# Optimization experiments

Measured on AMD Instinct MI355X. Metric: run time of the kernel, lower is better.

## Reference

```python
import jax, jax.numpy as jnp
import numpy as np

N, E = 50000, 800000
IN, HID, HEADS, OUT, EDIM = 128, 32, 4, 40, 5
HC = HEADS * HID  # 128, conv1 output width


def setup_inputs() -> dict:
    key = jax.random.key(0)
    ks = jax.random.split(key, 24)
    p = lambda i, shape: (jax.random.normal(ks[i], shape, jnp.float32) * 0.1)
    return {
        "x": jax.random.normal(ks[0], (N, IN), jnp.float32),
        "edge_index": jax.random.randint(ks[1], (2, E), 0, N, jnp.int32),
        "edge_attr": jax.random.normal(ks[2], (E, EDIM), jnp.float32),
        # GATConv layer 1 (in -> hidden, heads=4)
        "W1": p(3, (IN, HC)), "att_src1": p(4, (HEADS, HID)), "att_dst1": p(5, (HEADS, HID)),
        "att_edge1": p(6, (HEADS, HID)), "We1": p(7, (EDIM, HC)), "b1": p(8, (HC,)),
        # GATConv layer 2 (hidden*heads -> out, heads=1)
        "W2": p(9, (HC, OUT)), "att_src2": p(10, (1, OUT)), "att_dst2": p(11, (1, OUT)),
        "att_edge2": p(12, (1, OUT)), "We2": p(13, (EDIM, OUT)), "b2": p(14, (OUT,)),
        # BatchNorm (eval mode: running stats)
        "g1": jnp.ones((HC,), jnp.float32), "be1": p(15, (HC,)),
        "rm1": p(16, (HC,)), "rv1": jnp.ones((HC,), jnp.float32),
        "g2": jnp.ones((OUT,), jnp.float32), "be2": p(17, (OUT,)),
        "rm2": p(18, (OUT,)), "rv2": jnp.ones((OUT,), jnp.float32),
    }


def gat_conv(x, src, dst, eattr, W, a_src, a_dst, a_edge, We, b, H, C):
    n = x.shape[0]
    xs = (x @ W).reshape(n, H, C)                       # shared lin for src/dst (PyG)
    alpha_s = jnp.einsum('nhc,hc->nh', xs, a_src)       # [N,H]
    alpha_d = jnp.einsum('nhc,hc->nh', xs, a_dst)       # [N,H]
    e = (eattr @ We).reshape(-1, H, C)                  # [E',H,C]
    alpha_e = jnp.einsum('ehc,hc->eh', e, a_edge)       # [E',H]
    alpha = jax.nn.leaky_relu(alpha_s[src] + alpha_d[dst] + alpha_e, 0.2)
    # segment softmax over incoming edges of each dst node
    amax = jax.ops.segment_max(alpha, dst, num_segments=n)
    ex = jnp.exp(alpha - amax[dst])
    denom = jax.ops.segment_sum(ex, dst, num_segments=n)
    coef = ex / (denom[dst] + 1e-16)                    # [E',H]
    out = jax.ops.segment_sum(xs[src] * coef[:, :, None], dst, num_segments=n)
    return out.reshape(n, H * C) + b                    # concat heads + bias


def batch_norm_eval(x, g, be, rm, rv):
    return g * (x - rm) * jax.lax.rsqrt(rv + 1e-5) + be


def reference(x, edge_index, edge_attr, W1, att_src1, att_dst1, att_edge1, We1, b1,
              W2, att_src2, att_dst2, att_edge2, We2, b2,
              g1, be1, rm1, rv1, g2, be2, rm2, rv2):
    src0, dst0 = edge_index[0], edge_index[1]
    # add self loops with fill_value='mean': loop edge_attr = mean of incoming edge_attr
    cnt = jax.ops.segment_sum(jnp.ones((E,), x.dtype), dst0, num_segments=N)
    loop_attr = jax.ops.segment_sum(edge_attr, dst0, num_segments=N) / jnp.maximum(cnt, 1.0)[:, None]
    loop = jnp.arange(N, dtype=src0.dtype)
    src = jnp.concatenate([src0, loop])
    dst = jnp.concatenate([dst0, loop])
    ea = jnp.concatenate([edge_attr, loop_attr], axis=0)
    # layer 1 (dropout = identity in eval)
    h = gat_conv(x, src, dst, ea, W1, att_src1, att_dst1, att_edge1, We1, b1, HEADS, HID)
    h = jax.nn.elu(batch_norm_eval(h, g1, be1, rm1, rv1))
    # layer 2 (heads=1)
    h = gat_conv(h, src, dst, ea, W2, att_src2, att_dst2, att_edge2, We2, b2, 1, OUT)
    h = batch_norm_eval(h, g2, be2, rm2, rv2)
    return jax.nn.log_softmax(h, axis=1)
```

## Files before the change

kernel.cpp:

```cpp
#include <hip/hip_runtime.h>
#include <hip/hip_bf16.h>

#define NN 50000
#define NE 800000
#define SCAN_NB ((NN + 255) / 256)
#define G1_NB ((NN + 63) / 64)
#define A1_NB ((NN + 3) / 4)

typedef float f32x4_t __attribute__((ext_vector_type(4)));
typedef float f32x2_t __attribute__((ext_vector_type(2)));
typedef short s16x8_t __attribute__((ext_vector_type(8)));

__device__ __forceinline__ unsigned f2bf2(float a, float b) {
    unsigned ua = __float_as_uint(a);
    ua = (ua + 0x7fffu + ((ua >> 16) & 1u)) >> 16;
    unsigned ub = __float_as_uint(b);
    ub = (ub + 0x7fffu + ((ub >> 16) & 1u)) >> 16;
    return ua | (ub << 16);
}
__device__ __forceinline__ float bf_lo(unsigned u) { return __uint_as_float(u << 16); }
__device__ __forceinline__ float bf_hi(unsigned u) { return __uint_as_float(u & 0xffff0000u); }
__device__ __forceinline__ f32x2_t bfpair(unsigned u) {
    return (f32x2_t){__uint_as_float(u << 16), __uint_as_float(u & 0xffff0000u)};
}

__global__ __launch_bounds__(256) void prep_kernel(
    const float* __restrict__ We1, const float* __restrict__ ae1w,
    const float* __restrict__ We2, const float* __restrict__ ae2w,
    const float* __restrict__ W1, const float* __restrict__ W2,
    float* __restrict__ wf1, float* __restrict__ wf2,
    unsigned* __restrict__ w1t, unsigned* __restrict__ w2t,
    int* __restrict__ cnt) {
    int t = threadIdx.x;
    int g = blockIdx.x * 256 + t;
    if (g < NN) cnt[g] = 0;
    if (blockIdx.x != 0) return;
    if (t < 20) {
        int j = t >> 2, h = t & 3;
        float s = 0.f;
        for (int c = 0; c < 32; ++c) s += We1[j * 128 + h * 32 + c] * ae1w[h * 32 + c];
        wf1[j * 4 + h] = s;
    }
    if (t >= 32 && t < 37) {
        int j = t - 32;
        float s = 0.f;
        for (int c = 0; c < 40; ++c) s += We2[j * 40 + c] * ae2w[c];
        wf2[j] = s;
    }
    for (int i = t; i < 128 * 64; i += 256) {
        int c = i >> 6, kp = i & 63;
        w1t[i] = f2bf2(W1[(size_t)(2 * kp) * 128 + c], W1[(size_t)(2 * kp + 1) * 128 + c]);
    }
    for (int i = t; i < 48 * 64; i += 256) {
        int c = i >> 6, kp = i & 63;
        w2t[i] = (c < 40) ? f2bf2(W2[(size_t)(2 * kp) * 40 + c], W2[(size_t)(2 * kp + 1) * 40 + c]) : 0u;
    }
}

__global__ __launch_bounds__(256) void gemm1_count(
    const float* __restrict__ A, const unsigned* __restrict__ w1t,
    unsigned* __restrict__ out, const int* __restrict__ dst0,
    int* __restrict__ cnt, int* __restrict__ rank) {
    int t = threadIdx.x;
    int ebase = blockIdx.x * 1024 + t;
    int e0 = ebase, e1 = ebase + 256, e2 = ebase + 512, e3 = ebase + 768;
    int r0 = 0, r1 = 0, r2 = 0, r3 = 0;
    if (e0 < NE) r0 = atomicAdd(&cnt[dst0[e0]], 1);
    if (e1 < NE) r1 = atomicAdd(&cnt[dst0[e1]], 1);
    if (e2 < NE) r2 = atomicAdd(&cnt[dst0[e2]], 1);
    if (e3 < NE) r3 = atomicAdd(&cnt[dst0[e3]], 1);

    __shared__ unsigned sA[64 * 68];
    __shared__ unsigned sB[128 * 68];
    int row0 = blockIdx.x * 64;
    for (int i = t; i < 64 * 32; i += 256) {
        int r = i >> 5, q = i & 31;
        int gr = row0 + r;
        float4 v = (gr < NN) ? *(const float4*)&A[(size_t)gr * 128 + q * 4]
                             : make_float4(0.f, 0.f, 0.f, 0.f);
        sA[r * 68 + q * 2]     = f2bf2(v.x, v.y);
        sA[r * 68 + q * 2 + 1] = f2bf2(v.z, v.w);
    }
    for (int i = t; i < 128 * 16; i += 256) {
        int c = i >> 4, q = i & 15;
        *(uint4*)&sB[c * 68 + q * 4] = *(const uint4*)&w1t[c * 64 + q * 4];
    }
    __syncthreads();
    int wv = t >> 6, lane = t & 63;
    int lr = lane & 15, kgrp = lane >> 4;
    f32x4_t acc[8];
#pragma unroll
    for (int i = 0; i < 8; ++i) acc[i] = (f32x4_t){0.f, 0.f, 0.f, 0.f};
    int arow = wv * 16 + lr;
#pragma unroll
    for (int kt = 0; kt < 4; ++kt) {
        int kw = kt * 16 + kgrp * 4;
        s16x8_t af = *(const s16x8_t*)&sA[arow * 68 + kw];
#pragma unroll
        for (int tc = 0; tc < 8; ++tc) {
            s16x8_t bf = *(const s16x8_t*)&sB[(tc * 16 + lr) * 68 + kw];
            acc[tc] = __builtin_amdgcn_mfma_f32_16x16x32_bf16(af, bf, acc[tc], 0, 0, 0);
        }
    }
    int orow0 = row0 + wv * 16 + kgrp * 4;
#pragma unroll
    for (int tc = 0; tc < 8; ++tc) {
#pragma unroll
        for (int r = 0; r < 4; ++r) {
            float v = acc[tc][r];
            float other = __shfl_xor(v, 1);
            int gr = orow0 + r;
            if (!(lane & 1) && gr < NN)
                out[(size_t)gr * 64 + tc * 8 + (lr >> 1)] = f2bf2(v, other);
        }
    }
    if (e0 < NE) rank[e0] = r0;
    if (e1 < NE) rank[e1] = r1;
    if (e2 < NE) rank[e2] = r2;
    if (e3 < NE) rank[e3] = r3;
}

__global__ __launch_bounds__(256) void scan1_alpha1(
    const int* __restrict__ cnt, int* __restrict__ off, int* __restrict__ bsum,
    const unsigned* __restrict__ xs1u, const float* __restrict__ asw,
    const float* __restrict__ adw, float* __restrict__ as1, float* __restrict__ ad1) {
    if (blockIdx.x < SCAN_NB) {
        __shared__ int tmp[256];
        int t = threadIdx.x;
        int g = blockIdx.x * 256 + t;
        int v = (g < NN) ? cnt[g] : 0;
        tmp[t] = v;
        __syncthreads();
#pragma unroll
        for (int d = 1; d < 256; d <<= 1) {
            int u = (t >= d) ? tmp[t - d] : 0;
            __syncthreads();
            tmp[t] += u;
            __syncthreads();
        }
        if (g < NN) off[g] = tmp[t] - v;
        if (t == 255) bsum[blockIdx.x] = tmp[255];
        return;
    }
    int wid = ((blockIdx.x - SCAN_NB) * 256 + threadIdx.x) >> 6;
    if (wid >= NN) return;
    int lane = threadIdx.x & 63;
    int c = lane * 2;
    unsigned u = xs1u[(size_t)wid * 64 + lane];
    float vx = bf_lo(u), vy = bf_hi(u);
    float pa = vx * asw[c] + vy * asw[c + 1];
    float pd = vx * adw[c] + vy * adw[c + 1];
#pragma unroll
    for (int d = 8; d >= 1; d >>= 1) {
        pa += __shfl_xor(pa, d, 16);
        pd += __shfl_xor(pd, d, 16);
    }
    if ((lane & 15) == 0) {
        as1[wid * 4 + (lane >> 4)] = pa;
        ad1[wid * 4 + (lane >> 4)] = pd;
    }
}

__global__ __launch_bounds__(256) void scan3_kernel(int* __restrict__ off,
                                                    const int* __restrict__ bsum,
                                                    const int* __restrict__ cnt) {
    __shared__ int tmp[256];
    int t = threadIdx.x;
    int v = (t < SCAN_NB) ? bsum[t] : 0;
    tmp[t] = v;
    __syncthreads();
#pragma unroll
    for (int d = 1; d < 256; d <<= 1) {
        int u = (t >= d) ? tmp[t - d] : 0;
        __syncthreads();
        tmp[t] += u;
        __syncthreads();
    }
    int pre = (blockIdx.x == 0) ? 0 : tmp[blockIdx.x - 1];
    int g = blockIdx.x * 256 + t;
    if (g < NN) {
        int o = off[g] + pre;
        off[g] = o;
        if (g == NN - 1) off[NN] = o + cnt[g];
    }
}

__global__ __launch_bounds__(256) void fill_fold_kernel(
    const int* __restrict__ src0, const int* __restrict__ dst0,
    const float* __restrict__ eattr, const float* __restrict__ wf1,
    const float* __restrict__ wf2, const int* __restrict__ off,
    const int* __restrict__ rank, uint4* __restrict__ epk) {
    int base = blockIdx.x * 1024 + threadIdx.x;
#pragma unroll
    for (int k = 0; k < 4; ++k) {
        int e = base + k * 256;
        if (e >= NE) continue;
        float a[5];
#pragma unroll
        for (int j = 0; j < 5; ++j) a[j] = eattr[(size_t)e * 5 + j];
        float o[4];
#pragma unroll
        for (int h = 0; h < 4; ++h) {
            float s = 0.f;
#pragma unroll
            for (int j = 0; j < 5; ++j) s += a[j] * wf1[j * 4 + h];
            o[h] = s;
        }
        float s2 = 0.f;
#pragma unroll
        for (int j = 0; j < 5; ++j) s2 += a[j] * wf2[j];
        int pos = off[dst0[e]] + rank[e];
        epk[pos] = make_uint4((unsigned)src0[e], f2bf2(o[0], o[1]), f2bf2(o[2], o[3]),
                              __float_as_uint(s2));
    }
}

__global__ __launch_bounds__(256) void gat1_kernel(
    const uint4* __restrict__ epk, const int* __restrict__ off,
    const unsigned* __restrict__ xs1u,
    const float4* __restrict__ as1, const float4* __restrict__ ad1,
    const float* __restrict__ b1, const float* __restrict__ g1, const float* __restrict__ be1,
    const float* __restrict__ rm1, const float* __restrict__ rv1, unsigned* __restrict__ h1u) {
    __shared__ int   lds_s[4][4][16];
    __shared__ float lds_w[4][4][16][4];
    int wave = threadIdx.x >> 6;
    int lane = threadIdx.x & 63;
    int g = lane >> 4;
    int lr = lane & 15;
    int qh = lr >> 2;
    int n = blockIdx.x * 16 + wave * 4 + g;
    int e0 = off[n];
    int deg = off[n + 1] - e0;
    float4 adn = ad1[n];
    float4 asn = as1[n];
    f32x2_t acc2[4];
#pragma unroll
    for (int k = 0; k < 4; ++k) acc2[k] = (f32x2_t){0.f, 0.f};
    float ds0 = 0.f, ds1 = 0.f, ds2 = 0.f, ds3 = 0.f;
    float s0 = 0.f, s1 = 0.f, s2 = 0.f, s3 = 0.f;
    int mc = (deg + 15) >> 4;
    mc = max(mc, __shfl_xor(mc, 16));
    mc = max(mc, __shfl_xor(mc, 32));

    for (int ch = 0; ch < mc; ++ch) {
        int i = ch * 16 + lr;
        int s = 0;
        float w0 = 0.f, w1 = 0.f, w2 = 0.f, w3 = 0.f;
        if (i < deg) {
            uint4 ep = epk[e0 + i];
            s = (int)ep.x;
            float ax = bf_lo(ep.y), ay = bf_hi(ep.y);
            float az = bf_lo(ep.z), aw = bf_hi(ep.z);
            float4 av = as1[s];
            float a0 = av.x + adn.x + ax;
            float a1 = av.y + adn.y + ay;
            float a2 = av.z + adn.z + az;
            float a3 = av.w + adn.w + aw;
            a0 = a0 >= 0.f ? a0 : 0.2f * a0;
            a1 = a1 >= 0.f ? a1 : 0.2f * a1;
            a2 = a2 >= 0.f ? a2 : 0.2f * a2;
            a3 = a3 >= 0.f ? a3 : 0.2f * a3;
            w0 = __expf(a0); w1 = __expf(a1); w2 = __expf(a2); w3 = __expf(a3);
            ds0 += w0; ds1 += w1; ds2 += w2; ds3 += w3;
            s0 += ax; s1 += ay; s2 += az; s3 += aw;
        }
        lds_s[wave][g][lr] = s;
        *(float4*)&lds_w[wave][g][lr][0] = make_float4(w0, w1, w2, w3);
        __builtin_amdgcn_wave_barrier();
        int cn = deg - ch * 16;
        cn = cn > 16 ? 16 : (cn < 0 ? 0 : cn);
        int cnr = (cn + 7) & ~7;
        for (int j = 0; j < cnr; j += 8) {
            int sj[8];
            float ww[8];
            uint4 uu[8];
#pragma unroll
            for (int q2 = 0; q2 < 8; ++q2) {
                sj[q2] = lds_s[wave][g][j + q2];
                ww[q2] = lds_w[wave][g][j + q2][qh];
            }
#pragma unroll
            for (int q2 = 0; q2 < 8; ++q2)
                uu[q2] = *(const uint4*)&xs1u[(size_t)sj[q2] * 64 + lr * 4];
#pragma unroll
            for (int q2 = 0; q2 < 8; ++q2) {
                f32x2_t W = {ww[q2], ww[q2]};
                acc2[0] += W * bfpair(uu[q2].x);
                acc2[1] += W * bfpair(uu[q2].y);
                acc2[2] += W * bfpair(uu[q2].z);
                acc2[3] += W * bfpair(uu[q2].w);
            }
        }
        __builtin_amdgcn_wave_barrier();
    }
#pragma unroll
    for (int d = 8; d >= 1; d >>= 1) {
        ds0 += __shfl_xor(ds0, d, 16); ds1 += __shfl_xor(ds1, d, 16);
        ds2 += __shfl_xor(ds2, d, 16); ds3 += __shfl_xor(ds3, d, 16);
        s0 += __shfl_xor(s0, d, 16);   s1 += __shfl_xor(s1, d, 16);
        s2 += __shfl_xor(s2, d, 16);   s3 += __shfl_xor(s3, d, 16);
    }
    float invd = 1.f / fmaxf((float)deg, 1.f);
    float aL0 = asn.x + adn.x + s0 * invd;
    float aL1 = asn.y + adn.y + s1 * invd;
    float aL2 = asn.z + adn.z + s2 * invd;
    float aL3 = asn.w + adn.w + s3 * invd;
    aL0 = aL0 >= 0.f ? aL0 : 0.2f * aL0;
    aL1 = aL1 >= 0.f ? aL1 : 0.2f * aL1;
    aL2 = aL2 >= 0.f ? aL2 : 0.2f * aL2;
    aL3 = aL3 >= 0.f ? aL3 : 0.2f * aL3;
    float ws0 = __expf(aL0), ws1 = __expf(aL1), ws2 = __expf(aL2), ws3 = __expf(aL3);
    float wself = qh == 0 ? ws0 : (qh == 1 ? ws1 : (qh == 2 ? ws2 : ws3));
    float dh = qh == 0 ? ds0 + ws0 : (qh == 1 ? ds1 + ws1 : (qh == 2 ? ds2 + ws2 : ds3 + ws3));
    uint4 us = *(const uint4*)&xs1u[(size_t)n * 64 + lr * 4];
    f32x2_t Ws = {wself, wself};
    acc2[0] += Ws * bfpair(us.x); acc2[1] += Ws * bfpair(us.y);
    acc2[2] += Ws * bfpair(us.z); acc2[3] += Ws * bfpair(us.w);
    float inv = 1.f / (dh + 1e-16f);
    int c = lr * 8;
    uint4 ou;
    unsigned* op = (unsigned*)&ou;
#pragma unroll
    for (int k2 = 0; k2 < 4; ++k2) {
        int c0 = c + 2 * k2, c1 = c + 2 * k2 + 1;
        float o0 = acc2[k2][0] * inv + b1[c0];
        float o1 = acc2[k2][1] * inv + b1[c1];
        float sc0 = g1[c0] * rsqrtf(rv1[c0] + 1e-5f);
        float sc1 = g1[c1] * rsqrtf(rv1[c1] + 1e-5f);
        o0 = (o0 - rm1[c0]) * sc0 + be1[c0];
        o1 = (o1 - rm1[c1]) * sc1 + be1[c1];
        o0 = o0 > 0.f ? o0 : __expf(o0) - 1.f;
        o1 = o1 > 0.f ? o1 : __expf(o1) - 1.f;
        op[k2] = f2bf2(o0, o1);
    }
    *(uint4*)&h1u[(size_t)n * 64 + lr * 4] = ou;
}

__global__ __launch_bounds__(256) void gemm2_mfma(
    const unsigned* __restrict__ A, const unsigned* __restrict__ w2t,
    unsigned* __restrict__ out) {
    __shared__ unsigned sA[64 * 68];
    __shared__ unsigned sB[48 * 68];
    int t = threadIdx.x;
    int row0 = blockIdx.x * 64;
    for (int i = t; i < 64 * 16; i += 256) {
        int r = i >> 4, q = i & 15;
        int gr = row0 + r;
        uint4 v = (gr < NN) ? *(const uint4*)&A[(size_t)gr * 64 + q * 4]
                            : make_uint4(0u, 0u, 0u, 0u);
        *(uint4*)&sA[r * 68 + q * 4] = v;
    }
    for (int i = t; i < 48 * 16; i += 256) {
        int c = i >> 4, q = i & 15;
        *(uint4*)&sB[c * 68 + q * 4] = *(const uint4*)&w2t[c * 64 + q * 4];
    }
    __syncthreads();
    int wv = t >> 6, lane = t & 63;
    int lr = lane & 15, kgrp = lane >> 4;
    f32x4_t acc[3];
#pragma unroll
    for (int i = 0; i < 3; ++i) acc[i] = (f32x4_t){0.f, 0.f, 0.f, 0.f};
    int arow = wv * 16 + lr;
#pragma unroll
    for (int kt = 0; kt < 4; ++kt) {
        int kw = kt * 16 + kgrp * 4;
        s16x8_t af = *(const s16x8_t*)&sA[arow * 68 + kw];
#pragma unroll
        for (int tc = 0; tc < 3; ++tc) {
            s16x8_t bf = *(const s16x8_t*)&sB[(tc * 16 + lr) * 68 + kw];
            acc[tc] = __builtin_amdgcn_mfma_f32_16x16x32_bf16(af, bf, acc[tc], 0, 0, 0);
        }
    }
    int orow0 = row0 + wv * 16 + kgrp * 4;
#pragma unroll
    for (int tc = 0; tc < 3; ++tc) {
#pragma unroll
        for (int r = 0; r < 4; ++r) {
            float v = acc[tc][r];
            float other = __shfl_xor(v, 1);
            int gr = orow0 + r;
            if (!(lane & 1) && gr < NN && (tc < 2 || lr < 8))
                out[(size_t)gr * 32 + tc * 8 + (lr >> 1)] = f2bf2(v, other);
        }
    }
}

__global__ __launch_bounds__(256) void alpha2_kernel(
    const unsigned* __restrict__ xs2u, const float* __restrict__ asw,
    const float* __restrict__ adw, float* __restrict__ as2, float* __restrict__ ad2) {
    int wid = (blockIdx.x * 256 + threadIdx.x) >> 6;
    if (wid >= NN) return;
    int lane = threadIdx.x & 63;
    float pa = 0.f, pd = 0.f;
    if (lane < 20) {
        unsigned u = xs2u[(size_t)wid * 32 + lane];
        float vx = bf_lo(u), vy = bf_hi(u);
        int c = lane * 2;
        pa = vx * asw[c] + vy * asw[c + 1];
        pd = vx * adw[c] + vy * adw[c + 1];
    }
#pragma unroll
    for (int d = 16; d >= 1; d >>= 1) {
        pa += __shfl_xor(pa, d, 32);
        pd += __shfl_xor(pd, d, 32);
    }
    if (lane == 0) { as2[wid] = pa; ad2[wid] = pd; }
}

__global__ __launch_bounds__(256) void gat2_kernel(
    const uint4* __restrict__ epk, const int* __restrict__ off,
    const unsigned* __restrict__ xs2u,
    const float* __restrict__ as2, const float* __restrict__ ad2,
    const float* __restrict__ b2, const float* __restrict__ g2, const float* __restrict__ be2,
    const float* __restrict__ rm2, const float* __restrict__ rv2, float* __restrict__ outp) {
    __shared__ int   lds_s[4][72];
    __shared__ float lds_w[4][72];
    int wid = (blockIdx.x * 256 + threadIdx.x) >> 6;
    if (wid >= NN) return;
    int lane = threadIdx.x & 63;
    int warp = threadIdx.x >> 6;
    int n = wid;
    int e0 = off[n], e1 = off[n + 1];
    int deg = e1 - e0;
    int grp3 = lane / 20;
    int col = lane - grp3 * 20;
    bool act = grp3 < 3;
    int grpo = act ? grp3 : 0;
    if (lane < 8) {
        lds_s[warp][64 + lane] = 0;
        lds_w[warp][64 + lane] = 0.f;
    }
    float adn = ad2[n];
    float asn = as2[n];
    f32x2_t acc2 = {0.f, 0.f};
    float dsum = 0.f, aesum = 0.f;

    for (int base = 0; base < deg; base += 64) {
        int i = base + lane;
        int cn = min(64, deg - base);
        int s = 0;
        float w = 0.f;
        if (i < deg) {
            uint4 ep = epk[e0 + i];
            s = (int)ep.x;
            float ae = __uint_as_float(ep.w);
            float a = as2[s] + adn + ae;
            a = a >= 0.f ? a : 0.2f * a;
            w = __expf(a);
            dsum += w;
            aesum += ae;
        }
        lds_s[warp][lane] = s;
        lds_w[warp][lane] = w;
        __builtin_amdgcn_wave_barrier();
        int cnr = ((cn + 11) / 12) * 12;
        for (int j = 0; j < cnr; j += 12) {
            int jj0 = j + grpo, jj1 = jj0 + 3, jj2 = jj0 + 6, jj3 = jj0 + 9;
            int sj0 = lds_s[warp][jj0];
            int sj1 = lds_s[warp][jj1];
            int sj2 = lds_s[warp][jj2];
            int sj3 = lds_s[warp][jj3];
            float w0 = act ? lds_w[warp][jj0] : 0.f;
            float w1 = act ? lds_w[warp][jj1] : 0.f;
            float w2 = act ? lds_w[warp][jj2] : 0.f;
            float w3 = act ? lds_w[warp][jj3] : 0.f;
            unsigned u0 = xs2u[(size_t)sj0 * 32 + col];
            unsigned u1 = xs2u[(size_t)sj1 * 32 + col];
            unsigned u2 = xs2u[(size_t)sj2 * 32 + col];
            unsigned u3 = xs2u[(size_t)sj3 * 32 + col];
            acc2 += (f32x2_t){w0, w0} * bfpair(u0);
            acc2 += (f32x2_t){w1, w1} * bfpair(u1);
            acc2 += (f32x2_t){w2, w2} * bfpair(u2);
            acc2 += (f32x2_t){w3, w3} * bfpair(u3);
        }
        __builtin_amdgcn_wave_barrier();
    }
    {
        float p0 = __shfl(acc2[0], (lane + 20) & 63);
        float p1 = __shfl(acc2[1], (lane + 20) & 63);
        float q0 = __shfl(acc2[0], (lane + 40) & 63);
        float q1 = __shfl(acc2[1], (lane + 40) & 63);
        acc2[0] += p0 + q0;
        acc2[1] += p1 + q1;
    }
#pragma unroll
    for (int d = 32; d >= 1; d >>= 1) {
        dsum += __shfl_xor(dsum, d);
        aesum += __shfl_xor(aesum, d);
    }
    float invd = 1.f / fmaxf((float)deg, 1.f);
    float aL = asn + adn + aesum * invd;
    aL = aL >= 0.f ? aL : 0.2f * aL;
    float wself = __expf(aL);
    float denom = dsum + wself;

    float v0 = 0.f, v1 = 0.f;
    if (lane < 20) {
        unsigned u = xs2u[(size_t)n * 32 + lane];
        acc2[0] += wself * bf_lo(u);
        acc2[1] += wself * bf_hi(u);
        int c = lane * 2;
        float inv = 1.f / (denom + 1e-16f);
        v0 = acc2[0] * inv + b2[c];
        v1 = acc2[1] * inv + b2[c + 1];
        float sc0 = g2[c] * rsqrtf(rv2[c] + 1e-5f);
        float sc1 = g2[c + 1] * rsqrtf(rv2[c + 1] + 1e-5f);
        v0 = (v0 - rm2[c]) * sc0 + be2[c];
        v1 = (v1 - rm2[c + 1]) * sc1 + be2[c + 1];
    }
    float mx = (lane < 20) ? fmaxf(v0, v1) : -3.0e38f;
#pragma unroll
    for (int d = 32; d >= 1; d >>= 1) mx = fmaxf(mx, __shfl_xor(mx, d));
    float ex = (lane < 20) ? __expf(v0 - mx) + __expf(v1 - mx) : 0.f;
#pragma unroll
    for (int d = 32; d >= 1; d >>= 1) ex += __shfl_xor(ex, d);
    if (lane < 20) {
        float ls = __logf(ex);
        *(float2*)&outp[(size_t)n * 40 + lane * 2] = make_float2(v0 - mx - ls, v1 - mx - ls);
    }
}

extern "C" void kernel_launch(void* const* d_in, const int* in_sizes, int n_in,
                              void* d_out, int out_size, void* d_ws, size_t ws_size,
                              hipStream_t stream) {
    const float* x     = (const float*)d_in[0];
    const int*   ei    = (const int*)d_in[1];
    const float* eattr = (const float*)d_in[2];
    const float* W1    = (const float*)d_in[3];
    const float* as1w  = (const float*)d_in[4];
    const float* ad1w  = (const float*)d_in[5];
    const float* ae1w  = (const float*)d_in[6];
    const float* We1   = (const float*)d_in[7];
    const float* b1    = (const float*)d_in[8];
    const float* W2    = (const float*)d_in[9];
    const float* as2w  = (const float*)d_in[10];
    const float* ad2w  = (const float*)d_in[11];
    const float* ae2w  = (const float*)d_in[12];
    const float* We2   = (const float*)d_in[13];
    const float* b2    = (const float*)d_in[14];
    const float* g1    = (const float*)d_in[15];
    const float* be1   = (const float*)d_in[16];
    const float* rm1   = (const float*)d_in[17];
    const float* rv1   = (const float*)d_in[18];
    const float* g2    = (const float*)d_in[19];
    const float* be2   = (const float*)d_in[20];
    const float* rm2   = (const float*)d_in[21];
    const float* rv2   = (const float*)d_in[22];

    const int* src0 = ei;
    const int* dst0 = ei + NE;

    char* p = (char*)d_ws;
    auto take = [&](size_t nbytes) {
        void* r = (void*)p;
        p += (nbytes + 255) & ~(size_t)255;
        return r;
    };
    float*    wf1    = (float*)take(80);
    float*    wf2    = (float*)take(20);
    unsigned* w1t    = (unsigned*)take((size_t)128 * 64 * 4);
    unsigned* w2t    = (unsigned*)take((size_t)48 * 64 * 4);
    int*      cnt    = (int*)take((size_t)NN * 4);
    int*      off    = (int*)take((size_t)(NN + 1) * 4);
    int*      bsum   = (int*)take((size_t)SCAN_NB * 4);
    int*      rank   = (int*)take((size_t)NE * 4);
    uint4*    epk    = (uint4*)take((size_t)NE * 16);
    float*    as1    = (float*)take((size_t)NN * 16);
    float*    ad1    = (float*)take((size_t)NN * 16);
    float*    as2    = (float*)take((size_t)NN * 4);
    float*    ad2    = (float*)take((size_t)NN * 4);
    unsigned* xs1u   = (unsigned*)take((size_t)NN * 256);
    unsigned* h1u    = (unsigned*)take((size_t)NN * 256);
    unsigned* xs2u   = (unsigned*)take((size_t)NN * 128);

    prep_kernel<<<SCAN_NB, 256, 0, stream>>>(We1, ae1w, We2, ae2w, W1, W2, wf1, wf2,
                                             w1t, w2t, cnt);
    gemm1_count<<<G1_NB, 256, 0, stream>>>(x, w1t, xs1u, dst0, cnt, rank);
    scan1_alpha1<<<SCAN_NB + A1_NB, 256, 0, stream>>>(cnt, off, bsum, xs1u, as1w, ad1w,
                                                      as1, ad1);
    scan3_kernel<<<SCAN_NB, 256, 0, stream>>>(off, bsum, cnt);
    fill_fold_kernel<<<(NE + 1023) / 1024, 256, 0, stream>>>(src0, dst0, eattr, wf1, wf2,
                                                             off, rank, epk);
    gat1_kernel<<<NN / 16, 256, 0, stream>>>(epk, off, xs1u, (const float4*)as1,
                                             (const float4*)ad1, b1, g1, be1, rm1, rv1, h1u);
    gemm2_mfma<<<(NN + 63) / 64, 256, 0, stream>>>(h1u, w2t, xs2u);
    alpha2_kernel<<<(NN + 3) / 4, 256, 0, stream>>>(xs2u, as2w, ad2w, as2, ad2);
    gat2_kernel<<<(NN + 3) / 4, 256, 0, stream>>>(epk, off, xs2u, as2, ad2,
                                                  b2, g2, be2, rm2, rv2, (float*)d_out);
}
```

Measured before the change: 175.5 us.

## Replicate degree counters per XCC and split counting from gemm1

Degree counting now uses one counter array per XCC, chosen from the hardware XCC ID register. Each array is updated with relaxed workgroup-scope atomics, so the atomics stay in that XCC's L2 instead of going device-wide. The scan combines the replicas into per-node totals and per-XCC prefix offsets, and the fill kernel uses those offsets to place each edge. Counting moves out of the GEMM into its own kernel. The cost is an extra launch, zeroing eight counter arrays, and an extra prefix array, and correctness depends on workgroup-scope atomics being coherent within one XCC's L2.

```diff
diff --git a/kernel.cpp b/kernel.cpp
--- a/kernel.cpp
+++ b/kernel.cpp
@@ -6,6 +6,7 @@
 #define SCAN_NB ((NN + 255) / 256)
 #define G1_NB ((NN + 63) / 64)
 #define A1_NB ((NN + 3) / 4)
+#define NXCC 8
 
 typedef float f32x4_t __attribute__((ext_vector_type(4)));
 typedef float f32x2_t __attribute__((ext_vector_type(2)));
@@ -30,10 +31,13 @@
     const float* __restrict__ W1, const float* __restrict__ W2,
     float* __restrict__ wf1, float* __restrict__ wf2,
     unsigned* __restrict__ w1t, unsigned* __restrict__ w2t,
-    int* __restrict__ cnt) {
+    int* __restrict__ cnt_rep) {
     int t = threadIdx.x;
     int g = blockIdx.x * 256 + t;
-    if (g < NN) cnt[g] = 0;
+    if (g < NN) {
+#pragma unroll
+        for (int k = 0; k < NXCC; ++k) cnt_rep[(size_t)k * NN + g] = 0;
+    }
     if (blockIdx.x != 0) return;
     if (t < 20) {
         int j = t >> 2, h = t & 3;
@@ -57,21 +61,31 @@
     }
 }
 
-__global__ __launch_bounds__(256) void gemm1_count(
+__global__ __launch_bounds__(256) void count_kernel(const int* __restrict__ dst0,
+                                                    int* __restrict__ cnt_rep,
+                                                    int* __restrict__ rank) {
+    unsigned xcc;
+    asm volatile("s_getreg_b32 %0, hwreg(HW_REG_XCC_ID)" : "=s"(xcc));
+    xcc &= (NXCC - 1);
+    int* myc = cnt_rep + (size_t)xcc * NN;
+    int base = blockIdx.x * 1024 + threadIdx.x;
+#pragma unroll
+    for (int k = 0; k < 4; ++k) {
+        int e = base + k * 256;
+        if (e < NE) {
+            int r = __hip_atomic_fetch_add(&myc[dst0[e]], 1, __ATOMIC_RELAXED,
+                                           __HIP_MEMORY_SCOPE_WORKGROUP);
+            rank[e] = (int)((xcc << 24) | (unsigned)r);
+        }
+    }
+}
+
+__global__ __launch_bounds__(256) void gemm1_mfma(
     const float* __restrict__ A, const unsigned* __restrict__ w1t,
-    unsigned* __restrict__ out, const int* __restrict__ dst0,
-    int* __restrict__ cnt, int* __restrict__ rank) {
-    int t = threadIdx.x;
-    int ebase = blockIdx.x * 1024 + t;
-    int e0 = ebase, e1 = ebase + 256, e2 = ebase + 512, e3 = ebase + 768;
-    int r0 = 0, r1 = 0, r2 = 0, r3 = 0;
-    if (e0 < NE) r0 = atomicAdd(&cnt[dst0[e0]], 1);
-    if (e1 < NE) r1 = atomicAdd(&cnt[dst0[e1]], 1);
-    if (e2 < NE) r2 = atomicAdd(&cnt[dst0[e2]], 1);
-    if (e3 < NE) r3 = atomicAdd(&cnt[dst0[e3]], 1);
-
+    unsigned* __restrict__ out) {
     __shared__ unsigned sA[64 * 68];
     __shared__ unsigned sB[128 * 68];
+    int t = threadIdx.x;
     int row0 = blockIdx.x * 64;
     for (int i = t; i < 64 * 32; i += 256) {
         int r = i >> 5, q = i & 31;
@@ -114,21 +128,31 @@
                 out[(size_t)gr * 64 + tc * 8 + (lr >> 1)] = f2bf2(v, other);
         }
     }
-    if (e0 < NE) rank[e0] = r0;
-    if (e1 < NE) rank[e1] = r1;
-    if (e2 < NE) rank[e2] = r2;
-    if (e3 < NE) rank[e3] = r3;
 }
 
 __global__ __launch_bounds__(256) void scan1_alpha1(
-    const int* __restrict__ cnt, int* __restrict__ off, int* __restrict__ bsum,
+    const int* __restrict__ cnt_rep, int* __restrict__ off, int* __restrict__ bsum,
+    int* __restrict__ rpre, int* __restrict__ ctot,
     const unsigned* __restrict__ xs1u, const float* __restrict__ asw,
     const float* __restrict__ adw, float* __restrict__ as1, float* __restrict__ ad1) {
     if (blockIdx.x < SCAN_NB) {
         __shared__ int tmp[256];
         int t = threadIdx.x;
         int g = blockIdx.x * 256 + t;
-        int v = (g < NN) ? cnt[g] : 0;
+        int v = 0;
+        if (g < NN) {
+            int pre[NXCC];
+            int tot = 0;
+#pragma unroll
+            for (int k = 0; k < NXCC; ++k) {
+                pre[k] = tot;
+                tot += cnt_rep[(size_t)k * NN + g];
+            }
+            *(int4*)&rpre[(size_t)g * 8]     = make_int4(pre[0], pre[1], pre[2], pre[3]);
+            *(int4*)&rpre[(size_t)g * 8 + 4] = make_int4(pre[4], pre[5], pre[6], pre[7]);
+            ctot[g] = tot;
+            v = tot;
+        }
         tmp[t] = v;
         __syncthreads();
 #pragma unroll
@@ -163,7 +187,7 @@
 
 __global__ __launch_bounds__(256) void scan3_kernel(int* __restrict__ off,
                                                     const int* __restrict__ bsum,
-                                                    const int* __restrict__ cnt) {
+                                                    const int* __restrict__ ctot) {
     __shared__ int tmp[256];
     int t = threadIdx.x;
     int v = (t < SCAN_NB) ? bsum[t] : 0;
@@ -181,7 +205,7 @@
     if (g < NN) {
         int o = off[g] + pre;
         off[g] = o;
-        if (g == NN - 1) off[NN] = o + cnt[g];
+        if (g == NN - 1) off[NN] = o + ctot[g];
     }
 }
 
@@ -189,7 +213,8 @@
     const int* __restrict__ src0, const int* __restrict__ dst0,
     const float* __restrict__ eattr, const float* __restrict__ wf1,
     const float* __restrict__ wf2, const int* __restrict__ off,
-    const int* __restrict__ rank, uint4* __restrict__ epk) {
+    const int* __restrict__ rank, const int* __restrict__ rpre,
+    uint4* __restrict__ epk) {
     int base = blockIdx.x * 1024 + threadIdx.x;
 #pragma unroll
     for (int k = 0; k < 4; ++k) {
@@ -209,7 +234,9 @@
         float s2 = 0.f;
 #pragma unroll
         for (int j = 0; j < 5; ++j) s2 += a[j] * wf2[j];
-        int pos = off[dst0[e]] + rank[e];
+        int d = dst0[e];
+        unsigned rk = (unsigned)rank[e];
+        int pos = off[d] + rpre[(size_t)d * 8 + (rk >> 24)] + (int)(rk & 0xFFFFFFu);
         epk[pos] = make_uint4((unsigned)src0[e], f2bf2(o[0], o[1]), f2bf2(o[2], o[3]),
                               __float_as_uint(s2));
     }
@@ -556,31 +583,34 @@
         p += (nbytes + 255) & ~(size_t)255;
         return r;
     };
-    float*    wf1    = (float*)take(80);
-    float*    wf2    = (float*)take(20);
-    unsigned* w1t    = (unsigned*)take((size_t)128 * 64 * 4);
-    unsigned* w2t    = (unsigned*)take((size_t)48 * 64 * 4);
-    int*      cnt    = (int*)take((size_t)NN * 4);
-    int*      off    = (int*)take((size_t)(NN + 1) * 4);
-    int*      bsum   = (int*)take((size_t)SCAN_NB * 4);
-    int*      rank   = (int*)take((size_t)NE * 4);
-    uint4*    epk    = (uint4*)take((size_t)NE * 16);
-    float*    as1    = (float*)take((size_t)NN * 16);
-    float*    ad1    = (float*)take((size_t)NN * 16);
-    float*    as2    = (float*)take((size_t)NN * 4);
-    float*    ad2    = (float*)take((size_t)NN * 4);
-    unsigned* xs1u   = (unsigned*)take((size_t)NN * 256);
-    unsigned* h1u    = (unsigned*)take((size_t)NN * 256);
-    unsigned* xs2u   = (unsigned*)take((size_t)NN * 128);
+    float*    wf1     = (float*)take(80);
+    float*    wf2     = (float*)take(20);
+    unsigned* w1t     = (unsigned*)take((size_t)128 * 64 * 4);
+    unsigned* w2t     = (unsigned*)take((size_t)48 * 64 * 4);
+    int*      cnt_rep = (int*)take((size_t)NXCC * NN * 4);
+    int*      off     = (int*)take((size_t)(NN + 1) * 4);
+    int*      bsum    = (int*)take((size_t)SCAN_NB * 4);
+    int*      rpre    = (int*)take((size_t)NN * 8 * 4);
+    int*      ctot    = (int*)take((size_t)NN * 4);
+    int*      rank    = (int*)take((size_t)NE * 4);
+    uint4*    epk     = (uint4*)take((size_t)NE * 16);
+    float*    as1     = (float*)take((size_t)NN * 16);
+    float*    ad1     = (float*)take((size_t)NN * 16);
+    float*    as2     = (float*)take((size_t)NN * 4);
+    float*    ad2     = (float*)take((size_t)NN * 4);
+    unsigned* xs1u    = (unsigned*)take((size_t)NN * 256);
+    unsigned* h1u     = (unsigned*)take((size_t)NN * 256);
+    unsigned* xs2u    = (unsigned*)take((size_t)NN * 128);
 
     prep_kernel<<<SCAN_NB, 256, 0, stream>>>(We1, ae1w, We2, ae2w, W1, W2, wf1, wf2,
-                                             w1t, w2t, cnt);
-    gemm1_count<<<G1_NB, 256, 0, stream>>>(x, w1t, xs1u, dst0, cnt, rank);
-    scan1_alpha1<<<SCAN_NB + A1_NB, 256, 0, stream>>>(cnt, off, bsum, xs1u, as1w, ad1w,
-                                                      as1, ad1);
-    scan3_kernel<<<SCAN_NB, 256, 0, stream>>>(off, bsum, cnt);
+                                             w1t, w2t, cnt_rep);
+    count_kernel<<<(NE + 1023) / 1024, 256, 0, stream>>>(dst0, cnt_rep, rank);
+    gemm1_mfma<<<G1_NB, 256, 0, stream>>>(x, w1t, xs1u);
+    scan1_alpha1<<<SCAN_NB + A1_NB, 256, 0, stream>>>(cnt_rep, off, bsum, rpre, ctot,
+                                                      xs1u, as1w, ad1w, as1, ad1);
+    scan3_kernel<<<SCAN_NB, 256, 0, stream>>>(off, bsum, ctot);
     fill_fold_kernel<<<(NE + 1023) / 1024, 256, 0, stream>>>(src0, dst0, eattr, wf1, wf2,
-                                                             off, rank, epk);
+                                                             off, rank, rpre, epk);
     gat1_kernel<<<NN / 16, 256, 0, stream>>>(epk, off, xs1u, (const float4*)as1,
                                              (const float4*)ad1, b1, g1, be1, rm1, rv1, h1u);
     gemm2_mfma<<<(NN + 63) / 64, 256, 0, stream>>>(h1u, w2t, xs2u);
```

Measured after the change: 179.8 us. +2.5%, slower.
